# Performance work log

Measured on AMD Instinct MI355X. Metric: run time of the kernel, lower is better.

Reference implementation:

```python
import jax, jax.numpy as jnp
import numpy as np

HEADS = 8
DIM_HEAD = 64

def setup_inputs() -> dict:
    key = jax.random.key(0)
    k1, k2 = jax.random.split(key)
    x = jax.random.normal(k1, (4, 2048, 512), dtype=jnp.float32)
    W_qkv = jax.random.normal(k2, (512, 3 * HEADS * DIM_HEAD), dtype=jnp.float32) * (512 ** -0.5)
    return {"x": x, "W_qkv": W_qkv}

def reference(x, W_qkv):
    b, n, _ = x.shape
    h, d = HEADS, DIM_HEAD
    scale = d ** -0.5
    qkv = x @ W_qkv                                   # [b, n, 3*h*d]
    q, k, v = jnp.split(qkv, 3, axis=-1)
    # 'b n (h d) -> b h n d'
    q = q.reshape(b, n, h, d).transpose(0, 2, 1, 3)
    k = k.reshape(b, n, h, d).transpose(0, 2, 1, 3)
    v = v.reshape(b, n, h, d).transpose(0, 2, 1, 3)
    scores = jnp.einsum('bhid,bhjd->bhij', q, k) * scale
    attn_w = jax.nn.softmax(scores, axis=-1)
    out = jnp.einsum('bhij,bhjd->bhid', attn_w, v)
    # 'b h i d -> b i (h d)'
    return out.transpose(0, 2, 1, 3).reshape(b, n, h * d)
```

## Files before the change

kernel.cpp:

```cpp
#include <hip/hip_runtime.h>

#define BATCH 4
#define NSEQ  2048
#define DMODEL 512
#define NHEAD 8
#define DHEAD 64
#define NQKV  1536

typedef __bf16 bf16x8 __attribute__((ext_vector_type(8)));
typedef __bf16 bf16x4 __attribute__((ext_vector_type(4)));
typedef float  f32x4  __attribute__((ext_vector_type(4)));
typedef short  s16x4  __attribute__((ext_vector_type(4)));

__device__ inline void async16(const __bf16* g, __bf16* l) {
    __builtin_amdgcn_global_load_lds(
        (const __attribute__((address_space(1))) void*)g,
        (__attribute__((address_space(3))) void*)l, 16, 0, 0);
}

__device__ inline bf16x8 cvt8(const float* __restrict__ p) {
    float4 a = *(const float4*)p;
    float4 b = *(const float4*)(p + 4);
    bf16x8 r;
    r[0] = (__bf16)a.x; r[1] = (__bf16)a.y; r[2] = (__bf16)a.z; r[3] = (__bf16)a.w;
    r[4] = (__bf16)b.x; r[5] = (__bf16)b.y; r[6] = (__bf16)b.z; r[7] = (__bf16)b.w;
    return r;
}

__device__ inline f32x4 mfma_pv(s16x4 a, s16x4 b, f32x4 c) {
#if !defined(__HIP_DEVICE_COMPILE__)
    (void)a; (void)b;
    return c;
#elif __has_builtin(__builtin_amdgcn_mfma_f32_16x16x16bf16_1k)
    return __builtin_amdgcn_mfma_f32_16x16x16bf16_1k(a, b, c, 0, 0, 0);
#else
    bf16x4 a4 = __builtin_bit_cast(bf16x4, a);
    bf16x4 b4 = __builtin_bit_cast(bf16x4, b);
    bf16x8 a8 = {}, b8 = {};
    for (int i = 0; i < 4; ++i) { a8[i] = a4[i]; b8[i] = b4[i]; }
    return __builtin_amdgcn_mfma_f32_16x16x32_bf16(a8, b8, c, 0, 0, 0);
#endif
}

#define QSCALE 0.18033688011112042f

__global__ __launch_bounds__(256) void prep_kernel(
    const float* __restrict__ W, __bf16* __restrict__ Wt,
    const float* __restrict__ x, __bf16* __restrict__ xb) {
    const int tid = threadIdx.x;
    const int bi = blockIdx.x;
    if (bi >= 192) {
        int g = ((bi - 192) * 256 + tid) * 8;
        bf16x8 r = cvt8(&x[g]);
        *(bf16x8*)&xb[g] = r;
        return;
    }
    __shared__ __bf16 t[64][65];
    const int n0 = (bi % 24) * 64, k0 = (bi / 24) * 64;
    const int cr = tid >> 4;
    const int cc = (tid & 15) * 4;
    for (int p = 0; p < 4; ++p) {
        int r = p * 16 + cr;
        float4 v = *(const float4*)&W[(size_t)(k0 + r) * NQKV + n0 + cc];
        t[r][cc + 0] = (__bf16)v.x; t[r][cc + 1] = (__bf16)v.y;
        t[r][cc + 2] = (__bf16)v.z; t[r][cc + 3] = (__bf16)v.w;
    }
    __syncthreads();
    for (int p = 0; p < 4; ++p) {
        int r = p * 16 + cr;
        bf16x4 o = {t[cc + 0][r], t[cc + 1][r], t[cc + 2][r], t[cc + 3][r]};
        *(bf16x4*)&Wt[(size_t)(n0 + r) * DMODEL + k0 + cc] = o;
    }
}

__global__ __launch_bounds__(512) void qkv_gemm_kernel(
    const __bf16* __restrict__ xb, const __bf16* __restrict__ Wt,
    __bf16* __restrict__ Qw, __bf16* __restrict__ Kw, __bf16* __restrict__ Vw) {
    __shared__ __align__(16) char smem[49152];
    __bf16* Al = (__bf16*)smem;
    __bf16* Bl = Al + 16384;
    __bf16* T  = (__bf16*)smem;

    const int tid  = threadIdx.x;
    const int w    = tid >> 6;
    const int lane = tid & 63;
    const int quad = lane >> 4;
    const int l15  = lane & 15;
    const int wm   = w >> 1, wn = w & 1;
    const int m0 = blockIdx.x * 256;
    const int n0 = blockIdx.y * 128;
    const int segrow = lane >> 3;
    const int sc = (lane & 7) ^ segrow;

    f32x4 acc[4][4];
    for (int i = 0; i < 4; ++i)
        for (int j = 0; j < 4; ++j)
            acc[i][j] = (f32x4){0.f, 0.f, 0.f, 0.f};

    for (int kt = 0; kt < 8; ++kt) {
        const int k0 = kt * 64;
        for (int i = 0; i < 2; ++i) {
            int seg = w * 2 + i;
            int row = seg * 8 + segrow;
            async16(&Wt[(size_t)(n0 + row) * DMODEL + k0 + sc * 8], &Bl[seg * 512]);
        }
        for (int i = 0; i < 4; ++i) {
            int seg = w * 4 + i;
            int row = seg * 8 + segrow;
            async16(&xb[(size_t)(m0 + row) * DMODEL + k0 + sc * 8], &Al[seg * 512]);
        }
        __syncthreads();
        for (int kc = 0; kc < 2; ++kc) {
            bf16x8 af[4], bfr[4];
            for (int mb = 0; mb < 4; ++mb) {
                int row = wm * 64 + mb * 16 + l15;
                af[mb] = *(const bf16x8*)&Al[(row >> 3) * 512 +
                    ((row & 7) * 8 + ((kc * 4 + quad) ^ (row & 7))) * 8];
            }
            for (int nb = 0; nb < 4; ++nb) {
                int row = wn * 64 + nb * 16 + l15;
                bfr[nb] = *(const bf16x8*)&Bl[row * 64 + (((kc * 4 + quad) ^ (l15 & 7)) * 8)];
            }
            for (int mb = 0; mb < 4; ++mb)
                for (int nb = 0; nb < 4; ++nb)
                    acc[mb][nb] = __builtin_amdgcn_mfma_f32_16x16x32_bf16(
                        af[mb], bfr[nb], acc[mb][nb], 0, 0, 0);
        }
        __syncthreads();
    }

    const int which = n0 >> 9;
    const int bb  = m0 >> 11;
    const int nq0 = m0 & 2047;

    for (int ph = 0; ph < 2; ++ph) {
        if (which <= 1) {
            if ((wm >> 1) == ph)
                for (int mb = 0; mb < 4; ++mb)
                    for (int nb = 0; nb < 4; ++nb)
                        for (int r = 0; r < 4; ++r) {
                            int ml = (wm & 1) * 64 + mb * 16 + quad * 4 + r;
                            int nl = wn * 64 + nb * 16 + l15;
                            float a = acc[mb][nb][r];
                            if (which == 0) a *= QSCALE;
                            T[ml * 136 + nl] = (__bf16)a;
                        }
            __syncthreads();
            __bf16* dst = which ? Kw : Qw;
            const int h0 = (n0 & 511) >> 6;
            const int region = tid >> 8;
            const int bh = bb * NHEAD + h0 + region;
            __bf16* base = dst + ((size_t)bh * NSEQ + nq0 + ph * 128) * DHEAD;
            for (int i = 0; i < 4; ++i) {
                int chunk = (tid & 255) + i * 256;
                int f = chunk * 8;
                int ml = f >> 6, dd = f & 63;
                bf16x8 v = *(const bf16x8*)&T[ml * 136 + region * 64 + dd];
                *(bf16x8*)&base[ml * 64 + dd] = v;
            }
        } else {
            if ((wm >> 1) == ph)
                for (int mb = 0; mb < 4; ++mb)
                    for (int nb = 0; nb < 4; ++nb) {
                        int nl = wn * 64 + nb * 16 + l15;
                        int mlb = (wm & 1) * 64 + mb * 16 + quad * 4;
                        bf16x4 v = {(__bf16)acc[mb][nb][0], (__bf16)acc[mb][nb][1],
                                    (__bf16)acc[mb][nb][2], (__bf16)acc[mb][nb][3]};
                        *(bf16x4*)&T[nl * 136 + mlb] = v;
                    }
            __syncthreads();
            const int hv0 = ((n0 - 1024) & 511) >> 6;
            for (int i = 0; i < 4; ++i) {
                int gc = i * 512 + tid;
                int row = gc >> 4, ch = gc & 15;
                bf16x8 v = *(const bf16x8*)&T[row * 136 + ch * 8];
                int bh = bb * NHEAD + hv0 + (row >> 6);
                int dd = row & 63;
                *(bf16x8*)&Vw[((size_t)bh * DHEAD + dd) * NSEQ + nq0 + ph * 128 + ch * 8] = v;
            }
        }
        __syncthreads();
    }
}

__global__ __launch_bounds__(512) void attn_kernel(
    const __bf16* __restrict__ Qw, const __bf16* __restrict__ Kw,
    const __bf16* __restrict__ Vw, float* __restrict__ out) {
    __shared__ __align__(16) char smem[65536];
    float* Of = (float*)smem;

    const int tid  = threadIdx.x;
    const int w    = tid >> 6;
    const int wg   = w & 3;
    const int half = w >> 2;
    const int lane = tid & 63;
    const int quad = lane >> 4;
    const int l15  = lane & 15;
    const int bid  = blockIdx.x;
    const int rr   = bid & 31;
    const int bh   = (rr & 7) * 4 + (rr >> 3);
    const int qblk = bid >> 5;
    const int bb = bh >> 3, h = bh & 7;
    const int q0 = qblk * 128 + wg * 32;
    const int segrow = lane >> 3;
    const int sc = (lane & 7) ^ segrow;

    __bf16* HB = (__bf16*)smem + half * 16384;

    const __bf16* Qh = Qw + (size_t)bh * NSEQ * DHEAD;
    const __bf16* Kh = Kw + (size_t)bh * NSEQ * DHEAD;
    const __bf16* Vh = Vw + (size_t)bh * DHEAD * NSEQ;

    bf16x8 qf[2][2];
#pragma unroll
    for (int qb = 0; qb < 2; ++qb)
#pragma unroll
        for (int kc = 0; kc < 2; ++kc)
            qf[qb][kc] = *(const bf16x8*)&Qh[(size_t)(q0 + qb * 16 + l15) * DHEAD + kc * 32 + quad * 8];

    int offk[2][4], offv[4][4];
#pragma unroll
    for (int kc = 0; kc < 2; ++kc)
#pragma unroll
        for (int kb = 0; kb < 4; ++kb)
            offk[kc][kb] = (kb * 16 + l15) * 64 + (((kc * 4 + quad) ^ (l15 & 7)) * 8);
#pragma unroll
    for (int kb = 0; kb < 4; ++kb)
#pragma unroll
        for (int db = 0; db < 4; ++db) {
            int d = db * 16 + l15;
            int g = kb * 2 + (quad >> 1);
            offv[kb][db] = (d >> 3) * 512 + (d & 7) * 64 +
                           ((g ^ (d & 7)) * 8) + (quad & 1) * 4;
        }

    const f32x4 fzero = (f32x4){0.f, 0.f, 0.f, 0.f};

    f32x4 O[4][2];
    float l_st[2] = {0.f, 0.f};
#pragma unroll
    for (int db = 0; db < 4; ++db)
#pragma unroll
        for (int qb = 0; qb < 2; ++qb)
            O[db][qb] = fzero;

    auto stage = [&](int it, int b) {
        const int k0 = (half * 16 + it) * 64;
        __bf16* KL = HB + b * 8192;
        __bf16* VL = KL + 4096;
        for (int i = 0; i < 2; ++i) {
            int seg = wg * 2 + i;
            int row = seg * 8 + segrow;
            async16(&Kh[(size_t)(k0 + row) * DHEAD + sc * 8], &KL[seg * 512]);
            async16(&Vh[(size_t)row * NSEQ + k0 + sc * 8], &VL[seg * 512]);
        }
    };

    stage(0, 0);
    for (int it = 0; it < 16; ++it) {
        __syncthreads();
        if (it < 15) stage(it + 1, (it + 1) & 1);
        const __bf16* Kb = HB + (it & 1) * 8192;
        const __bf16* Vb = Kb + 4096;

        f32x4 s[4][2];
#pragma unroll
        for (int kc = 0; kc < 2; ++kc) {
            bf16x8 ak[4];
#pragma unroll
            for (int kb = 0; kb < 4; ++kb)
                ak[kb] = *(const bf16x8*)&Kb[offk[kc][kb]];
#pragma unroll
            for (int kb = 0; kb < 4; ++kb)
#pragma unroll
                for (int qb = 0; qb < 2; ++qb)
                    s[kb][qb] = __builtin_amdgcn_mfma_f32_16x16x32_bf16(
                        ak[kb], qf[qb][kc], kc == 0 ? fzero : s[kb][qb], 0, 0, 0);
        }

        s16x4 pb[4][2];
#pragma unroll
        for (int qb = 0; qb < 2; ++qb) {
            float rsum = 0.f;
#pragma unroll
            for (int kb = 0; kb < 4; ++kb) {
                bf16x4 t;
#pragma unroll
                for (int r = 0; r < 4; ++r) {
                    float p = __builtin_amdgcn_exp2f(s[kb][qb][r]);
                    rsum += p;
                    t[r] = (__bf16)p;
                }
                pb[kb][qb] = __builtin_bit_cast(s16x4, t);
            }
            l_st[qb] += rsum;
        }

#pragma unroll
        for (int kb = 0; kb < 4; ++kb) {
            s16x4 av[4];
#pragma unroll
            for (int db = 0; db < 4; ++db)
                av[db] = *(const s16x4*)&Vb[offv[kb][db]];
#pragma unroll
            for (int db = 0; db < 4; ++db)
#pragma unroll
                for (int qb = 0; qb < 2; ++qb)
                    O[db][qb] = mfma_pv(av[db], pb[kb][qb], O[db][qb]);
        }
    }

    for (int qb = 0; qb < 2; ++qb) {
        l_st[qb] += __shfl_xor(l_st[qb], 16);
        l_st[qb] += __shfl_xor(l_st[qb], 32);
    }

    __syncthreads();
    if (half == 0) {
        for (int qb = 0; qb < 2; ++qb) {
            int q = wg * 32 + qb * 16 + l15;
            for (int db = 0; db < 4; ++db)
                *(f32x4*)&Of[q * 68 + db * 16 + quad * 4] = O[db][qb];
            if (quad == 0) Of[q * 68 + 64] = l_st[qb];
        }
    }
    __syncthreads();
    if (half == 1) {
        for (int qb = 0; qb < 2; ++qb) {
            int q = wg * 32 + qb * 16 + l15;
            float inv = 1.f / (l_st[qb] + Of[q * 68 + 64]);
            for (int db = 0; db < 4; ++db) {
                f32x4 v = *(const f32x4*)&Of[q * 68 + db * 16 + quad * 4];
                v = (v + O[db][qb]) * inv;
                *(f32x4*)&Of[q * 68 + db * 16 + quad * 4] = v;
            }
        }
    }
    __syncthreads();
    const int nqb = qblk * 128;
    for (int i = 0; i < 4; ++i) {
        int gc = i * 512 + tid;
        int row = gc >> 4, ch = gc & 15;
        f32x4 v = *(const f32x4*)&Of[row * 68 + ch * 4];
        *(f32x4*)&out[((size_t)(bb * NSEQ + nqb + row)) * DMODEL + h * DHEAD + ch * 4] = v;
    }
}

extern "C" void kernel_launch(void* const* d_in, const int* in_sizes, int n_in,
                              void* d_out, int out_size, void* d_ws, size_t ws_size,
                              hipStream_t stream) {
    const float* x = (const float*)d_in[0];
    const float* W = (const float*)d_in[1];
    float* out = (float*)d_out;

    __bf16* wsp = (__bf16*)d_ws;
    __bf16* Wt = wsp;
    __bf16* Qw = Wt + 786432;
    __bf16* Kw = Qw + 4194304;
    __bf16* Vw = Kw + 4194304;
    __bf16* xb = Vw + 4194304;

    prep_kernel<<<2240, 256, 0, stream>>>(W, Wt, x, xb);
    qkv_gemm_kernel<<<dim3(32, 12), 512, 0, stream>>>(xb, Wt, Qw, Kw, Vw);
    attn_kernel<<<512, 512, 0, stream>>>(Qw, Kw, Vw, out);
}
```

Baseline: 130.3 us.

## Double-buffer QKV GEMM LDS tiles with K=32 stages to overlap loads

The QKV projection GEMM now uses two LDS buffers of K=32 slices and prefetches the next slice with async global-to-LDS loads while MFMAs run on the current one. It drops one barrier per iteration and replaces the 8-way XOR swizzle with a 4-way swizzle suited to 32-wide rows. The aim is to hide global load latency in the GEMM. In exchange there are twice as many loop iterations, each doing half the MFMA work, so barrier overhead per unit of compute grows, and the new swizzle may cause more LDS bank conflicts. Only the GEMM part of the total kernel time is affected.

```diff
diff --git a/kernel.cpp b/kernel.cpp
--- a/kernel.cpp
+++ b/kernel.cpp
@@ -89,45 +89,52 @@
     const int wm   = w >> 1, wn = w & 1;
     const int m0 = blockIdx.x * 256;
     const int n0 = blockIdx.y * 128;
-    const int segrow = lane >> 3;
-    const int sc = (lane & 7) ^ segrow;
+    const int srow  = lane >> 2;
+    const int sslot = lane & 3;
 
     f32x4 acc[4][4];
     for (int i = 0; i < 4; ++i)
         for (int j = 0; j < 4; ++j)
             acc[i][j] = (f32x4){0.f, 0.f, 0.f, 0.f};
 
-    for (int kt = 0; kt < 8; ++kt) {
-        const int k0 = kt * 64;
+    auto stage = [&](int kt, int b) {
+        const int k0 = kt * 32;
+        __bf16* AL = Al + b * 8192;
+        __bf16* BL = Bl + b * 4096;
+        {
+            int row = w * 16 + srow;
+            async16(&Wt[(size_t)(n0 + row) * DMODEL + k0 + ((sslot ^ (row & 3)) * 8)],
+                    &BL[w * 512]);
+        }
         for (int i = 0; i < 2; ++i) {
             int seg = w * 2 + i;
-            int row = seg * 8 + segrow;
-            async16(&Wt[(size_t)(n0 + row) * DMODEL + k0 + sc * 8], &Bl[seg * 512]);
-        }
-        for (int i = 0; i < 4; ++i) {
-            int seg = w * 4 + i;
-            int row = seg * 8 + segrow;
-            async16(&xb[(size_t)(m0 + row) * DMODEL + k0 + sc * 8], &Al[seg * 512]);
-        }
+            int row = seg * 16 + srow;
+            async16(&xb[(size_t)(m0 + row) * DMODEL + k0 + ((sslot ^ (row & 3)) * 8)],
+                    &AL[seg * 512]);
+        }
+    };
+
+    stage(0, 0);
+    for (int kt = 0; kt < 16; ++kt) {
         __syncthreads();
-        for (int kc = 0; kc < 2; ++kc) {
-            bf16x8 af[4], bfr[4];
-            for (int mb = 0; mb < 4; ++mb) {
-                int row = wm * 64 + mb * 16 + l15;
-                af[mb] = *(const bf16x8*)&Al[(row >> 3) * 512 +
-                    ((row & 7) * 8 + ((kc * 4 + quad) ^ (row & 7))) * 8];
-            }
-            for (int nb = 0; nb < 4; ++nb) {
-                int row = wn * 64 + nb * 16 + l15;
-                bfr[nb] = *(const bf16x8*)&Bl[row * 64 + (((kc * 4 + quad) ^ (l15 & 7)) * 8)];
-            }
-            for (int mb = 0; mb < 4; ++mb)
-                for (int nb = 0; nb < 4; ++nb)
-                    acc[mb][nb] = __builtin_amdgcn_mfma_f32_16x16x32_bf16(
-                        af[mb], bfr[nb], acc[mb][nb], 0, 0, 0);
-        }
-        __syncthreads();
-    }
+        if (kt < 15) stage(kt + 1, (kt + 1) & 1);
+        const __bf16* AL = Al + (kt & 1) * 8192;
+        const __bf16* BL = Bl + (kt & 1) * 4096;
+        bf16x8 af[4], bfr[4];
+        for (int mb = 0; mb < 4; ++mb) {
+            int row = wm * 64 + mb * 16 + l15;
+            af[mb] = *(const bf16x8*)&AL[row * 32 + ((quad ^ (row & 3)) * 8)];
+        }
+        for (int nb = 0; nb < 4; ++nb) {
+            int row = wn * 64 + nb * 16 + l15;
+            bfr[nb] = *(const bf16x8*)&BL[row * 32 + ((quad ^ (row & 3)) * 8)];
+        }
+        for (int mb = 0; mb < 4; ++mb)
+            for (int nb = 0; nb < 4; ++nb)
+                acc[mb][nb] = __builtin_amdgcn_mfma_f32_16x16x32_bf16(
+                    af[mb], bfr[nb], acc[mb][nb], 0, 0, 0);
+    }
+    __syncthreads();
 
     const int which = n0 >> 9;
     const int bb  = m0 >> 11;
```

New measurement: 137.4 us. +5.4%, slower.
